# Kernel optimization log

Measured on AMD Instinct MI355X. Metric: run time of the kernel, lower is better.

## Reference

```python
import jax, jax.numpy as jnp
import numpy as np

N, E, S, G = 20000, 60000, 3000, 128
EAD = 5
DIMS = [(16, 32), (32, 64), (64, 64)]  # NNConv (M_in, M_out) per layer
HID = 128  # edge-MLP hidden
FC_IN = 64 + 8  # conv output + raw continuous feats


def setup_inputs() -> dict:
    key = jax.random.key(0)
    ks = iter(jax.random.split(key, 64))
    inp = {}
    inp['x'] = jax.random.normal(next(ks), (N, 24), jnp.float32)
    inp['edge_index'] = jax.random.randint(next(ks), (2, E), 0, N)
    inp['edge_attr'] = jax.random.uniform(next(ks), (E, EAD), jnp.float32)
    inp['node_to_subgraph'] = jnp.sort(jax.random.randint(next(ks), (N,), 0, S))
    inp['subgraph_to_graph'] = jnp.sort(jax.random.randint(next(ks), (S,), 0, G))
    for i, (mi, mo) in enumerate(DIMS):
        inp[f'conv{i}_w1'] = jax.random.normal(next(ks), (EAD, HID), jnp.float32) / np.sqrt(EAD)
        inp[f'conv{i}_b1'] = jnp.zeros((HID,), jnp.float32)
        inp[f'conv{i}_w2'] = jax.random.normal(next(ks), (HID, mi * mo), jnp.float32) / np.sqrt(HID * mi)
        inp[f'conv{i}_b2'] = jnp.zeros((mi * mo,), jnp.float32)
        inp[f'conv{i}_root'] = jax.random.normal(next(ks), (mi, mo), jnp.float32) / np.sqrt(mi)
        inp[f'conv{i}_bias'] = jnp.zeros((mo,), jnp.float32)
    dims_fc = [(FC_IN, FC_IN // 2), (FC_IN // 2, FC_IN // 4), (FC_IN // 4, 1)]
    for i, (di, do) in enumerate(dims_fc):
        inp[f'fc{i+1}_w'] = jax.random.normal(next(ks), (di, do), jnp.float32) / np.sqrt(di)
        inp[f'fc{i+1}_b'] = jnp.zeros((do,), jnp.float32)
    return inp


def _nnconv(x, src, dst, ea, w1, b1, w2, b2, root, bias):
    # edge MLP -> per-edge weight matrix [E, M_in, M_out]
    h = jax.nn.relu(ea @ w1 + b1)
    mi, mo = root.shape
    W = (h @ w2 + b2).reshape(-1, mi, mo)
    msg = jnp.einsum('ei,eio->eo', x[src], W)  # gather + per-edge matmul
    agg = jax.ops.segment_sum(msg, dst, num_segments=x.shape[0])  # scatter-add
    return agg + x @ root + bias


def _mean_pool(x, seg, num):
    s = jax.ops.segment_sum(x, seg, num_segments=num)
    c = jax.ops.segment_sum(jnp.ones((x.shape[0], 1), x.dtype), seg, num_segments=num)
    return s / jnp.maximum(c, 1.0)


def _forward(x, edge_index, edge_attr, node_to_subgraph, subgraph_to_graph, convs, fcs):
    src, dst = edge_index[0], edge_index[1]
    xi = x[:, :16]
    for p in convs:
        xi = jax.nn.elu(_nnconv(xi, src, dst, edge_attr, *p))
    x_cont = x[:, 16:]
    xc = jnp.concatenate([xi, x_cont], axis=1)  # [N, 72]
    xs = _mean_pool(xc, node_to_subgraph, S)    # [S, 72]
    xg = _mean_pool(xs, subgraph_to_graph, G)   # [G, 72]
    (w1, b1), (w2, b2), (w3, b3) = fcs
    xg = jax.nn.elu(xg @ w1 + b1)
    xg = jax.nn.elu(xg @ w2 + b2)
    return (xg @ w3 + b3).reshape(-1)


def reference(x, edge_index, edge_attr, node_to_subgraph, subgraph_to_graph,
              conv0_w1, conv0_b1, conv0_w2, conv0_b2, conv0_root, conv0_bias,
              conv1_w1, conv1_b1, conv1_w2, conv1_b2, conv1_root, conv1_bias,
              conv2_w1, conv2_b1, conv2_w2, conv2_b2, conv2_root, conv2_bias,
              fc1_w, fc1_b, fc2_w, fc2_b, fc3_w, fc3_b):
    convs = [
        (conv0_w1, conv0_b1, conv0_w2, conv0_b2, conv0_root, conv0_bias),
        (conv1_w1, conv1_b1, conv1_w2, conv1_b2, conv1_root, conv1_bias),
        (conv2_w1, conv2_b1, conv2_w2, conv2_b2, conv2_root, conv2_bias),
    ]
    fcs = [(fc1_w, fc1_b), (fc2_w, fc2_b), (fc3_w, fc3_b)]
    return _forward(x, edge_index, edge_attr, node_to_subgraph, subgraph_to_graph, convs, fcs)
```

## Files before the change

kernel.cpp:

```cpp
#include <hip/hip_runtime.h>
#include <hip/hip_bf16.h>
#include <cmath>

#define NN 20000
#define NE 60000
#define NS 3000
#define NG 128
#define HIDN 128
#define SCB 79

typedef float f32x16 __attribute__((ext_vector_type(16)));
typedef _Float16 f16x8 __attribute__((ext_vector_type(8)));

__device__ __forceinline__ float eluf(float v) { return v > 0.f ? v : expm1f(v); }

__device__ __forceinline__ void gload_lds16(const void* g, void* l) {
    __builtin_amdgcn_global_load_lds(
        (const __attribute__((address_space(1))) unsigned int*)g,
        (__attribute__((address_space(3))) unsigned int*)l, 16, 0, 0);
}

__device__ __forceinline__ void vmwait0() {
    asm volatile("s_waitcnt vmcnt(0)" ::: "memory");
}
__device__ __forceinline__ void vmwait8() {
    asm volatile("s_waitcnt vmcnt(8)" ::: "memory");
}

__global__ void k_hist(const int* __restrict__ dst, int* __restrict__ deg) {
    int e = blockIdx.x * 256 + threadIdx.x;
    if (e < NE) atomicAdd(&deg[dst[e]], 1);
}

__global__ void k_scan1(const int* __restrict__ deg, int* __restrict__ bsum) {
    __shared__ int s[256];
    const int t = threadIdx.x;
    int i = blockIdx.x * 256 + t;
    s[t] = (i < NN) ? deg[i] : 0;
    __syncthreads();
#pragma unroll
    for (int off = 128; off > 0; off >>= 1) {
        if (t < off) s[t] += s[t + off];
        __syncthreads();
    }
    if (t == 0) bsum[blockIdx.x] = s[0];
}

__global__ void k_scan2(const int* __restrict__ bsum, int* __restrict__ boff) {
    __shared__ int s[SCB];
    const int t = threadIdx.x;
    if (t < SCB) s[t] = bsum[t];
    __syncthreads();
    if (t == 0) {
        int acc = 0;
        for (int i = 0; i < SCB; ++i) { int v = s[i]; s[i] = acc; acc += v; }
    }
    __syncthreads();
    if (t < SCB) boff[t] = s[t];
}

__global__ void k_scan3(const int* __restrict__ deg, const int* __restrict__ boff,
                        int* __restrict__ rowptr) {
    __shared__ int s[256];
    const int t = threadIdx.x;
    int i = blockIdx.x * 256 + t;
    int v = (i < NN) ? deg[i] : 0;
    s[t] = v;
    __syncthreads();
#pragma unroll
    for (int off = 1; off < 256; off <<= 1) {
        int a = (t >= off) ? s[t - off] : 0;
        __syncthreads();
        s[t] += a;
        __syncthreads();
    }
    if (i < NN) rowptr[i + 1] = boff[blockIdx.x] + s[t];
    if (i == 0) rowptr[0] = 0;
}

__global__ void k_scatter(const int* __restrict__ src, const int* __restrict__ dst,
                          const int* __restrict__ rowptr, int* __restrict__ tmp,
                          int* __restrict__ eord, int* __restrict__ srcS) {
    int e = blockIdx.x * 256 + threadIdx.x;
    if (e >= NE) return;
    int d = dst[e];
    int pos = rowptr[d] + atomicAdd(&tmp[d], 1);
    eord[pos] = e;
    srcS[pos] = src[e];
}

#define PRE_N0 66048
#define PRE_N1 264192
#define PRE_N2 528384
#define PRE_N3 320000
#define PRE_TOT (PRE_N0 + PRE_N1 + PRE_N2 + PRE_N3)

__global__ void k_prep(const float* __restrict__ w20, const float* __restrict__ b20,
                       const float* __restrict__ w21, const float* __restrict__ b21,
                       const float* __restrict__ w22, const float* __restrict__ b22,
                       const float* __restrict__ x,
                       _Float16* __restrict__ w2t0, _Float16* __restrict__ w2t1,
                       _Float16* __restrict__ w2t2, _Float16* __restrict__ x16h) {
    int idx = blockIdx.x * 256 + threadIdx.x;
    if (idx < PRE_N0) {
        constexpr int KP = 129 * 16, KF = 128 * 16, MO = 32;
        int o = idx / KP, kg = idx % KP;
        float v = (kg < KF) ? w20[(size_t)kg * MO + o] : b20[(kg - KF) * MO + o];
        w2t0[idx] = (_Float16)v;
    } else if (idx < PRE_N0 + PRE_N1) {
        int i2 = idx - PRE_N0;
        constexpr int KP = 129 * 32, KF = 128 * 32, MO = 64;
        int o = i2 / KP, kg = i2 % KP;
        float v = (kg < KF) ? w21[(size_t)kg * MO + o] : b21[(kg - KF) * MO + o];
        w2t1[i2] = (_Float16)v;
    } else if (idx < PRE_N0 + PRE_N1 + PRE_N2) {
        int i2 = idx - PRE_N0 - PRE_N1;
        constexpr int KP = 129 * 64, KF = 128 * 64, MO = 64;
        int o = i2 / KP, kg = i2 % KP;
        float v = (kg < KF) ? w22[(size_t)kg * MO + o] : b22[(kg - KF) * MO + o];
        w2t2[i2] = (_Float16)v;
    } else if (idx < PRE_TOT) {
        int i2 = idx - PRE_N0 - PRE_N1 - PRE_N2;
        int n = i2 >> 4, i = i2 & 15;
        x16h[i2] = (_Float16)x[n * 24 + i];
    }
}

template <int MI, int MO, int XS>
__global__ __launch_bounds__(256, 2) void k_edgeB(
    const _Float16* __restrict__ xi, const float* __restrict__ ea,
    const float* __restrict__ w1, const float* __restrict__ b1,
    const _Float16* __restrict__ w2t, const int* __restrict__ srcS,
    const int* __restrict__ eord, _Float16* __restrict__ msg) {
    constexpr int PH  = MI / 16;
    constexpr int KP  = 129 * MI;
    constexpr int NT  = MO / 32;
    constexpr int CH  = 16 / (PH * NT);
    constexpr int NCH = 64 / CH;
    static_assert(CH * PH * NT == 16, "ITEMS must be 16");
    static_assert(NCH % 2 == 0, "chunk loop unrolled x2");

    __shared__ __align__(16) _Float16 sb[2][2][16 * 512];

    const int lane = threadIdx.x & 63;
    const int w    = threadIdx.x >> 6;
    const int mg   = w & 1;
    const int kh   = w >> 1;
    const int lo5  = lane & 31;
    const int hi   = lane >> 5;
    const int e0   = blockIdx.x * 128 + mg * 64;
    const int kb   = kh * 64;

    const int rc0 = min(e0 + lo5, NE - 1);
    const int rc1 = min(e0 + 32 + lo5, NE - 1);
    const int s0 = srcS[rc0];
    const int s1 = srcS[rc1];

    float ea0[5], ea1[5];
    {
        const int eo0 = eord[rc0], eo1 = eord[rc1];
#pragma unroll
        for (int d = 0; d < 5; ++d) {
            ea0[d] = ea[eo0 * 5 + d];
            ea1[d] = ea[eo1 * 5 + d];
        }
    }

    f16x8 xr0[PH], xr1[PH];
    {
        const _Float16* xb0 = xi + (size_t)s0 * XS + hi * 8;
        const _Float16* xb1 = xi + (size_t)s1 * XS + hi * 8;
#pragma unroll
        for (int p = 0; p < PH; ++p) {
            xr0[p] = *reinterpret_cast<const f16x8*>(xb0 + p * 16);
            xr1[p] = *reinterpret_cast<const f16x8*>(xb1 + p * 16);
        }
    }

    f32x16 acc[2][NT];
#pragma unroll
    for (int m = 0; m < 2; ++m)
#pragma unroll
        for (int n = 0; n < NT; ++n)
#pragma unroll
            for (int i = 0; i < 16; ++i) acc[m][n][i] = 0.f;

    auto stage = [&](int buf, int kc) {
#pragma unroll
        for (int jj = 0; jj < 8; ++jj) {
            const int j  = mg + jj * 2;
            const int n  = j % NT;
            const int kp = j / NT;
            const int p  = kp % PH;
            const int kk = kp / PH;
            gload_lds16(w2t + (size_t)(n * 32 + lo5) * KP
                            + (size_t)(kb + kc + kk) * MI + p * 16 + hi * 8,
                        &sb[kh][buf][j * 512]);
        }
    };

    auto calc_h = [&](int kc, _Float16* h0, _Float16* h1) {
#pragma unroll
        for (int kk = 0; kk < CH; ++kk) {
            const int k = kb + kc + kk;
            const float c0 = w1[0 * HIDN + k], c1 = w1[1 * HIDN + k],
                        c2 = w1[2 * HIDN + k], c3 = w1[3 * HIDN + k],
                        c4 = w1[4 * HIDN + k], bb = b1[k];
            float t0 = bb, t1 = bb;
            t0 = fmaf(ea0[0], c0, t0); t1 = fmaf(ea1[0], c0, t1);
            t0 = fmaf(ea0[1], c1, t0); t1 = fmaf(ea1[1], c1, t1);
            t0 = fmaf(ea0[2], c2, t0); t1 = fmaf(ea1[2], c2, t1);
            t0 = fmaf(ea0[3], c3, t0); t1 = fmaf(ea1[3], c3, t1);
            t0 = fmaf(ea0[4], c4, t0); t1 = fmaf(ea1[4], c4, t1);
            h0[kk] = (_Float16)fmaxf(t0, 0.f);
            h1[kk] = (_Float16)fmaxf(t1, 0.f);
        }
    };

    auto compute = [&](int buf, const _Float16* h0, const _Float16* h1) {
        const _Float16* sbc = &sb[kh][buf][0];
#pragma unroll
        for (int kk = 0; kk < CH; ++kk) {
            const _Float16 hv0 = h0[kk];
            const _Float16 hv1 = h1[kk];
            const f16x8 h80 = {hv0, hv0, hv0, hv0, hv0, hv0, hv0, hv0};
            const f16x8 h81 = {hv1, hv1, hv1, hv1, hv1, hv1, hv1, hv1};
#pragma unroll
            for (int p = 0; p < PH; ++p) {
                const f16x8 af0 = xr0[p] * h80;
                const f16x8 af1 = xr1[p] * h81;
#pragma unroll
                for (int n = 0; n < NT; ++n) {
                    const f16x8 bv = *reinterpret_cast<const f16x8*>(
                        &sbc[((kk * PH + p) * NT + n) * 512 + lane * 8]);
                    acc[0][n] = __builtin_amdgcn_mfma_f32_32x32x16_f16(af0, bv, acc[0][n], 0, 0, 0);
                    acc[1][n] = __builtin_amdgcn_mfma_f32_32x32x16_f16(af1, bv, acc[1][n], 0, 0, 0);
                }
            }
        }
    };

    _Float16 hA0[CH], hA1[CH], hB0[CH], hB1[CH];

    stage(0, 0);
    calc_h(0, hA0, hA1);

    for (int c = 0; c < NCH; c += 2) {
        stage(1, (c + 1) * CH);
        calc_h((c + 1) * CH, hB0, hB1);
        vmwait8();
        __builtin_amdgcn_sched_barrier(0);
        __builtin_amdgcn_s_barrier();
        __builtin_amdgcn_sched_barrier(0);
        compute(0, hA0, hA1);
        __builtin_amdgcn_sched_barrier(0);
        __builtin_amdgcn_s_barrier();

        const bool pf = (c + 2 < NCH);
        if (pf) {
            stage(0, (c + 2) * CH);
            calc_h((c + 2) * CH, hA0, hA1);
            vmwait8();
        } else {
            vmwait0();
        }
        __builtin_amdgcn_sched_barrier(0);
        __builtin_amdgcn_s_barrier();
        __builtin_amdgcn_sched_barrier(0);
        compute(1, hB0, hB1);
        __builtin_amdgcn_sched_barrier(0);
        __builtin_amdgcn_s_barrier();
    }

    if (kh == 1) {
#pragma unroll
        for (int p = 0; p < PH; ++p) {
#pragma unroll
            for (int n = 0; n < NT; ++n) {
                const f16x8 bv = *reinterpret_cast<const f16x8*>(
                    w2t + (size_t)(n * 32 + lo5) * KP + (size_t)128 * MI + p * 16 + hi * 8);
                acc[0][n] = __builtin_amdgcn_mfma_f32_32x32x16_f16(xr0[p], bv, acc[0][n], 0, 0, 0);
                acc[1][n] = __builtin_amdgcn_mfma_f32_32x32x16_f16(xr1[p], bv, acc[1][n], 0, 0, 0);
            }
        }
    }

    __syncthreads();
    float* red = reinterpret_cast<float*>(&sb[0][0][0]);
    if (kh == 1) {
#pragma unroll
        for (int m = 0; m < 2; ++m)
#pragma unroll
            for (int n = 0; n < NT; ++n) {
                float* d = red + (size_t)((mg * 2 + m) * NT + n) * 1024 + lane;
#pragma unroll
                for (int i = 0; i < 16; ++i) d[i * 64] = acc[m][n][i];
            }
    }
    __syncthreads();
    if (kh == 0) {
#pragma unroll
        for (int m = 0; m < 2; ++m)
#pragma unroll
            for (int n = 0; n < NT; ++n) {
                const float* s = red + (size_t)((mg * 2 + m) * NT + n) * 1024 + lane;
#pragma unroll
                for (int i = 0; i < 16; ++i) acc[m][n][i] += s[i * 64];
            }
#pragma unroll
        for (int m = 0; m < 2; ++m)
#pragma unroll
            for (int q = 0; q < 4; ++q)
#pragma unroll
                for (int a2 = 0; a2 < 4; ++a2) {
                    const int e = e0 + m * 32 + 4 * hi + 8 * q + a2;
                    if (e < NE) {
#pragma unroll
                        for (int n = 0; n < NT; ++n)
                            msg[(size_t)e * MO + n * 32 + lo5] =
                                (_Float16)acc[m][n][4 * q + a2];
                    }
                }
    }
}

template <int MI, int MO, int XS>
__global__ void k_agg(const _Float16* __restrict__ msg, const int* __restrict__ rowptr,
                      const float* __restrict__ xi, const float* __restrict__ root,
                      const float* __restrict__ bias, float* __restrict__ out,
                      _Float16* __restrict__ outh) {
    int idx = blockIdx.x * 256 + threadIdx.x;
    if (idx >= NN * MO) return;
    int n = idx / MO, o = idx % MO;
    float s = bias[o];
#pragma unroll
    for (int i = 0; i < MI; ++i) s = fmaf(xi[(size_t)n * XS + i], root[i * MO + o], s);
    const int j0 = rowptr[n], j1 = rowptr[n + 1];
    for (int j = j0; j < j1; ++j) s += (float)msg[(size_t)j * MO + o];
    float r = eluf(s);
    out[idx] = r;
    outh[idx] = (_Float16)r;
}

__global__ void k_agg_pool(const _Float16* __restrict__ msg, const int* __restrict__ rowptr,
                           const float* __restrict__ xi, const float* __restrict__ root,
                           const float* __restrict__ bias, const float* __restrict__ x,
                           const int* __restrict__ n2s, float* __restrict__ xs_sum,
                           float* __restrict__ cs) {
    int idx = blockIdx.x * 256 + threadIdx.x;
    if (idx >= NN * 72) return;
    int n = idx / 72, o = idx % 72;
    float r;
    if (o < 64) {
        float s = bias[o];
#pragma unroll
        for (int i = 0; i < 64; ++i) s = fmaf(xi[(size_t)n * 64 + i], root[i * 64 + o], s);
        const int j0 = rowptr[n], j1 = rowptr[n + 1];
        for (int j = j0; j < j1; ++j) s += (float)msg[(size_t)j * 64 + o];
        r = eluf(s);
    } else {
        r = x[n * 24 + 16 + (o - 64)];
    }
    const int sg = n2s[n];
    atomicAdd(&xs_sum[sg * 72 + o], r);
    if (o == 0) atomicAdd(&cs[sg], 1.f);
}

__global__ void k_pool_g(const float* __restrict__ xs_sum, const float* __restrict__ cs,
                         const int* __restrict__ s2g, float* __restrict__ xg_sum,
                         float* __restrict__ cg) {
    int idx = blockIdx.x * 256 + threadIdx.x;
    if (idx >= NS * 72) return;
    int s = idx / 72, j = idx % 72;
    float v = xs_sum[s * 72 + j] / fmaxf(cs[s], 1.f);
    int g = s2g[s];
    atomicAdd(&xg_sum[g * 72 + j], v);
    if (j == 0) atomicAdd(&cg[g], 1.f);
}

__global__ void k_fc(const float* __restrict__ xg_sum, const float* __restrict__ cg,
                     const float* __restrict__ w1, const float* __restrict__ b1,
                     const float* __restrict__ w2, const float* __restrict__ b2,
                     const float* __restrict__ w3, const float* __restrict__ b3,
                     float* __restrict__ out) {
    int g = threadIdx.x;
    if (g >= NG) return;
    float inv = 1.f / fmaxf(cg[g], 1.f);
    float v[72];
#pragma unroll
    for (int j = 0; j < 72; ++j) v[j] = xg_sum[g * 72 + j] * inv;
    float h1[36];
#pragma unroll
    for (int o = 0; o < 36; ++o) {
        float s = b1[o];
#pragma unroll
        for (int i = 0; i < 72; ++i) s = fmaf(v[i], w1[i * 36 + o], s);
        h1[o] = eluf(s);
    }
    float h2[18];
#pragma unroll
    for (int o = 0; o < 18; ++o) {
        float s = b2[o];
#pragma unroll
        for (int i = 0; i < 36; ++i) s = fmaf(h1[i], w2[i * 18 + o], s);
        h2[o] = eluf(s);
    }
    float s = b3[0];
#pragma unroll
    for (int i = 0; i < 18; ++i) s = fmaf(h2[i], w3[i], s);
    out[g] = s;
}

extern "C" void kernel_launch(void* const* d_in, const int* in_sizes, int n_in,
                              void* d_out, int out_size, void* d_ws, size_t ws_size,
                              hipStream_t stream) {
    const float* x   = (const float*)d_in[0];
    const int*   ei  = (const int*)d_in[1];
    const float* ea  = (const float*)d_in[2];
    const int*   n2s = (const int*)d_in[3];
    const int*   s2g = (const int*)d_in[4];
    const int* src = ei;
    const int* dst = ei + NE;

    const float* cw1[3]   = {(const float*)d_in[5],  (const float*)d_in[11], (const float*)d_in[17]};
    const float* cb1[3]   = {(const float*)d_in[6],  (const float*)d_in[12], (const float*)d_in[18]};
    const float* cw2[3]   = {(const float*)d_in[7],  (const float*)d_in[13], (const float*)d_in[19]};
    const float* cb2[3]   = {(const float*)d_in[8],  (const float*)d_in[14], (const float*)d_in[20]};
    const float* croot[3] = {(const float*)d_in[9],  (const float*)d_in[15], (const float*)d_in[21]};
    const float* cbias[3] = {(const float*)d_in[10], (const float*)d_in[16], (const float*)d_in[22]};
    const float* fc1w = (const float*)d_in[23];
    const float* fc1b = (const float*)d_in[24];
    const float* fc2w = (const float*)d_in[25];
    const float* fc2b = (const float*)d_in[26];
    const float* fc3w = (const float*)d_in[27];
    const float* fc3b = (const float*)d_in[28];

    char* W = (char*)d_ws;
    float*    xiA   = (float*)(W);
    float*    xiB   = (float*)(W + 5120000);
    _Float16* xiAh  = (_Float16*)(W + 10240000);
    _Float16* xiBh  = (_Float16*)(W + 12800000);
    _Float16* x16h  = (_Float16*)(W + 15360000);
    _Float16* msg   = (_Float16*)(W + 16000000);
    float*    xs_sum= (float*)(W + 23680000);
    float*    cs    = (float*)(W + 24544000);
    float*    xg_sum= (float*)(W + 24556000);
    float*    cg    = (float*)(W + 24592864);
    int*      deg   = (int*)(W + 24593376);
    int*      tmp   = (int*)(W + 24673376);
    _Float16* w2t0  = (_Float16*)(W + 24753376);
    _Float16* w2t1  = (_Float16*)(W + 24885472);
    _Float16* w2t2  = (_Float16*)(W + 25413856);
    int*      rowptr= (int*)(W + 26470624);
    int*      eord  = (int*)(W + 26550640);
    int*      srcS  = (int*)(W + 26790640);
    int*      bsum  = (int*)(W + 27030640);
    int*      boff  = (int*)(W + 27030960);

    hipMemsetAsync(xs_sum, 0, 1073376, stream);

    k_hist<<<(NE + 255) / 256, 256, 0, stream>>>(dst, deg);
    k_scan1<<<SCB, 256, 0, stream>>>(deg, bsum);
    k_scan2<<<1, 128, 0, stream>>>(bsum, boff);
    k_scan3<<<SCB, 256, 0, stream>>>(deg, boff, rowptr);
    k_scatter<<<(NE + 255) / 256, 256, 0, stream>>>(src, dst, rowptr, tmp, eord, srcS);

    k_prep<<<(PRE_TOT + 255) / 256, 256, 0, stream>>>(
        cw2[0], cb2[0], cw2[1], cb2[1], cw2[2], cb2[2], x, w2t0, w2t1, w2t2, x16h);

    const int EB = (NE + 127) / 128;

    k_edgeB<16, 32, 16><<<EB, 256, 0, stream>>>(x16h, ea, cw1[0], cb1[0], w2t0, srcS, eord, msg);
    k_agg<16, 32, 24><<<(NN * 32 + 255) / 256, 256, 0, stream>>>(msg, rowptr, x, croot[0], cbias[0], xiB, xiBh);

    k_edgeB<32, 64, 32><<<EB, 256, 0, stream>>>(xiBh, ea, cw1[1], cb1[1], w2t1, srcS, eord, msg);
    k_agg<32, 64, 32><<<(NN * 64 + 255) / 256, 256, 0, stream>>>(msg, rowptr, xiB, croot[1], cbias[1], xiA, xiAh);

    k_edgeB<64, 64, 64><<<EB, 256, 0, stream>>>(xiAh, ea, cw1[2], cb1[2], w2t2, srcS, eord, msg);
    k_agg_pool<<<(NN * 72 + 255) / 256, 256, 0, stream>>>(msg, rowptr, xiA, croot[2], cbias[2],
                                                          x, n2s, xs_sum, cs);

    k_pool_g<<<(NS * 72 + 255) / 256, 256, 0, stream>>>(xs_sum, cs, s2g, xg_sum, cg);
    k_fc<<<1, 128, 0, stream>>>(xg_sum, cg, fc1w, fc1b, fc2w, fc2b, fc3w, fc3b, (float*)d_out);
}
```

Measured before the change: 302.0 us.

## Split layer-3 edge kernel over hidden-dim slices with partial message buffers

```diff
diff --git a/kernel.cpp b/kernel.cpp
--- a/kernel.cpp
+++ b/kernel.cpp
@@ -8,6 +8,8 @@
 #define NG 128
 #define HIDN 128
 #define SCB 79
+#define TILES 938
+#define SLST 3840000
 
 typedef float f32x16 __attribute__((ext_vector_type(16)));
 typedef _Float16 f16x8 __attribute__((ext_vector_type(8)));
@@ -325,6 +327,134 @@
 }
 
 template <int MI, int MO, int XS>
+__global__ __launch_bounds__(768, 3) void k_edgeP(
+    const _Float16* __restrict__ xi, const float* __restrict__ ea,
+    const float* __restrict__ w1, const float* __restrict__ b1,
+    const _Float16* __restrict__ w2t, const int* __restrict__ srcS,
+    const int* __restrict__ eord, _Float16* __restrict__ msgP, int tilesPerBlock) {
+    constexpr int PH = MI / 16;
+    constexpr int KP = 129 * MI;
+    constexpr int NT = MO / 32;
+    constexpr int MAXITEMS = 17 * PH * NT;
+
+    __shared__ __align__(16) _Float16 sb[MAXITEMS * 512];
+
+    const int t    = threadIdx.x;
+    const int lane = t & 63;
+    const int w    = t >> 6;
+    const int lo5  = lane & 31;
+    const int hi   = lane >> 5;
+
+    const int sl    = blockIdx.y;
+    const int k0    = sl * 16;
+    const int kspan = (sl == 7) ? 17 : 16;
+    const int items = kspan * PH * NT;
+
+    for (int j = w; j < items; j += 12) {
+        const int kk  = j / (PH * NT);
+        const int rem = j % (PH * NT);
+        const int p   = rem / NT;
+        const int n   = rem % NT;
+        gload_lds16(w2t + (size_t)(n * 32 + lo5) * KP
+                        + (size_t)(k0 + kk) * MI + p * 16 + hi * 8,
+                    &sb[j * 512]);
+    }
+    vmwait0();
+    __syncthreads();
+
+    _Float16* msgS = msgP + (size_t)sl * SLST;
+    const int tile0 = blockIdx.x * tilesPerBlock;
+    const int tile1 = min(tile0 + tilesPerBlock, TILES);
+
+    for (int tile = tile0 + w; tile < tile1; tile += 12) {
+        const int e0  = tile * 64;
+        const int rc0 = min(e0 + lo5, NE - 1);
+        const int rc1 = min(e0 + 32 + lo5, NE - 1);
+        const int s0 = srcS[rc0];
+        const int s1 = srcS[rc1];
+
+        float ea0[5], ea1[5];
+        {
+            const int eo0 = eord[rc0], eo1 = eord[rc1];
+#pragma unroll
+            for (int d = 0; d < 5; ++d) {
+                ea0[d] = ea[eo0 * 5 + d];
+                ea1[d] = ea[eo1 * 5 + d];
+            }
+        }
+
+        f16x8 xr0[PH], xr1[PH];
+        {
+            const _Float16* xb0 = xi + (size_t)s0 * XS + hi * 8;
+            const _Float16* xb1 = xi + (size_t)s1 * XS + hi * 8;
+#pragma unroll
+            for (int p = 0; p < PH; ++p) {
+                xr0[p] = *reinterpret_cast<const f16x8*>(xb0 + p * 16);
+                xr1[p] = *reinterpret_cast<const f16x8*>(xb1 + p * 16);
+            }
+        }
+
+        f32x16 acc[2][NT];
+#pragma unroll
+        for (int m = 0; m < 2; ++m)
+#pragma unroll
+            for (int n = 0; n < NT; ++n)
+#pragma unroll
+                for (int i = 0; i < 16; ++i) acc[m][n][i] = 0.f;
+
+        for (int kk2 = 0; kk2 < kspan; ++kk2) {
+            const int k = k0 + kk2;
+            _Float16 hv0, hv1;
+            if (k < 128) {
+                const float c0 = w1[0 * HIDN + k], c1 = w1[1 * HIDN + k],
+                            c2 = w1[2 * HIDN + k], c3 = w1[3 * HIDN + k],
+                            c4 = w1[4 * HIDN + k], bb = b1[k];
+                float t0 = bb, t1 = bb;
+                t0 = fmaf(ea0[0], c0, t0); t1 = fmaf(ea1[0], c0, t1);
+                t0 = fmaf(ea0[1], c1, t0); t1 = fmaf(ea1[1], c1, t1);
+                t0 = fmaf(ea0[2], c2, t0); t1 = fmaf(ea1[2], c2, t1);
+                t0 = fmaf(ea0[3], c3, t0); t1 = fmaf(ea1[3], c3, t1);
+                t0 = fmaf(ea0[4], c4, t0); t1 = fmaf(ea1[4], c4, t1);
+                hv0 = (_Float16)fmaxf(t0, 0.f);
+                hv1 = (_Float16)fmaxf(t1, 0.f);
+            } else {
+                hv0 = (_Float16)1.0f;
+                hv1 = (_Float16)1.0f;
+            }
+            const f16x8 h80 = {hv0, hv0, hv0, hv0, hv0, hv0, hv0, hv0};
+            const f16x8 h81 = {hv1, hv1, hv1, hv1, hv1, hv1, hv1, hv1};
+#pragma unroll
+            for (int p = 0; p < PH; ++p) {
+                const f16x8 af0 = xr0[p] * h80;
+                const f16x8 af1 = xr1[p] * h81;
+#pragma unroll
+                for (int n = 0; n < NT; ++n) {
+                    const f16x8 bv = *reinterpret_cast<const f16x8*>(
+                        &sb[((kk2 * PH + p) * NT + n) * 512 + lane * 8]);
+                    acc[0][n] = __builtin_amdgcn_mfma_f32_32x32x16_f16(af0, bv, acc[0][n], 0, 0, 0);
+                    acc[1][n] = __builtin_amdgcn_mfma_f32_32x32x16_f16(af1, bv, acc[1][n], 0, 0, 0);
+                }
+            }
+        }
+
+#pragma unroll
+        for (int m = 0; m < 2; ++m)
+#pragma unroll
+            for (int q = 0; q < 4; ++q)
+#pragma unroll
+                for (int a2 = 0; a2 < 4; ++a2) {
+                    const int e = e0 + m * 32 + 4 * hi + 8 * q + a2;
+                    if (e < NE) {
+#pragma unroll
+                        for (int n = 0; n < NT; ++n)
+                            msgS[(size_t)e * MO + n * 32 + lo5] =
+                                (_Float16)acc[m][n][4 * q + a2];
+                    }
+                }
+    }
+}
+
+template <int MI, int MO, int XS>
 __global__ void k_agg(const _Float16* __restrict__ msg, const int* __restrict__ rowptr,
                       const float* __restrict__ xi, const float* __restrict__ root,
                       const float* __restrict__ bias, float* __restrict__ out,
@@ -342,7 +472,8 @@
     outh[idx] = (_Float16)r;
 }
 
-__global__ void k_agg_pool(const _Float16* __restrict__ msg, const int* __restrict__ rowptr,
+__global__ void k_agg_pool(const _Float16* __restrict__ msgP, int nsl,
+                           const int* __restrict__ rowptr,
                            const float* __restrict__ xi, const float* __restrict__ root,
                            const float* __restrict__ bias, const float* __restrict__ x,
                            const int* __restrict__ n2s, float* __restrict__ xs_sum,
@@ -356,7 +487,10 @@
 #pragma unroll
         for (int i = 0; i < 64; ++i) s = fmaf(xi[(size_t)n * 64 + i], root[i * 64 + o], s);
         const int j0 = rowptr[n], j1 = rowptr[n + 1];
-        for (int j = j0; j < j1; ++j) s += (float)msg[(size_t)j * 64 + o];
+        for (int j = j0; j < j1; ++j) {
+            const _Float16* mp = msgP + (size_t)j * 64 + o;
+            for (int sl = 0; sl < nsl; ++sl) s += (float)mp[(size_t)sl * SLST];
+        }
         r = eluf(s);
     } else {
         r = x[n * 24 + 16 + (o - 64)];
@@ -441,21 +575,24 @@
     _Float16* xiAh  = (_Float16*)(W + 10240000);
     _Float16* xiBh  = (_Float16*)(W + 12800000);
     _Float16* x16h  = (_Float16*)(W + 15360000);
-    _Float16* msg   = (_Float16*)(W + 16000000);
-    float*    xs_sum= (float*)(W + 23680000);
-    float*    cs    = (float*)(W + 24544000);
-    float*    xg_sum= (float*)(W + 24556000);
-    float*    cg    = (float*)(W + 24592864);
-    int*      deg   = (int*)(W + 24593376);
-    int*      tmp   = (int*)(W + 24673376);
-    _Float16* w2t0  = (_Float16*)(W + 24753376);
-    _Float16* w2t1  = (_Float16*)(W + 24885472);
-    _Float16* w2t2  = (_Float16*)(W + 25413856);
-    int*      rowptr= (int*)(W + 26470624);
-    int*      eord  = (int*)(W + 26550640);
-    int*      srcS  = (int*)(W + 26790640);
-    int*      bsum  = (int*)(W + 27030640);
-    int*      boff  = (int*)(W + 27030960);
+    float*    xs_sum= (float*)(W + 16000000);
+    float*    cs    = (float*)(W + 16864000);
+    float*    xg_sum= (float*)(W + 16876000);
+    float*    cg    = (float*)(W + 16912864);
+    int*      deg   = (int*)(W + 16913376);
+    int*      tmp   = (int*)(W + 16993376);
+    _Float16* w2t0  = (_Float16*)(W + 17073376);
+    _Float16* w2t1  = (_Float16*)(W + 17205472);
+    _Float16* w2t2  = (_Float16*)(W + 17733856);
+    int*      rowptr= (int*)(W + 18790624);
+    int*      eord  = (int*)(W + 18870640);
+    int*      srcS  = (int*)(W + 19110640);
+    int*      bsum  = (int*)(W + 19350640);
+    int*      boff  = (int*)(W + 19350960);
+    _Float16* msgP  = (_Float16*)(W + 19351296);
+    const size_t NEED_P = 19351296ull + 8ull * 7680000ull;
+    const bool useP = (ws_size >= NEED_P);
+    _Float16* msg = msgP;
 
     hipMemsetAsync(xs_sum, 0, 1073376, stream);
 
@@ -476,9 +613,18 @@
     k_edgeB<32, 64, 32><<<EB, 256, 0, stream>>>(xiBh, ea, cw1[1], cb1[1], w2t1, srcS, eord, msg);
     k_agg<32, 64, 32><<<(NN * 64 + 255) / 256, 256, 0, stream>>>(msg, rowptr, xiB, croot[1], cbias[1], xiA, xiAh);
 
-    k_edgeB<64, 64, 64><<<EB, 256, 0, stream>>>(xiAh, ea, cw1[2], cb1[2], w2t2, srcS, eord, msg);
-    k_agg_pool<<<(NN * 72 + 255) / 256, 256, 0, stream>>>(msg, rowptr, xiA, croot[2], cbias[2],
-                                                          x, n2s, xs_sum, cs);
+    if (useP) {
+        const int XB = 32;
+        const int TPB = (TILES + XB - 1) / XB;
+        k_edgeP<64, 64, 64><<<dim3(XB, 8), 768, 0, stream>>>(
+            xiAh, ea, cw1[2], cb1[2], w2t2, srcS, eord, msgP, TPB);
+        k_agg_pool<<<(NN * 72 + 255) / 256, 256, 0, stream>>>(
+            msgP, 8, rowptr, xiA, croot[2], cbias[2], x, n2s, xs_sum, cs);
+    } else {
+        k_edgeB<64, 64, 64><<<EB, 256, 0, stream>>>(xiAh, ea, cw1[2], cb1[2], w2t2, srcS, eord, msg);
+        k_agg_pool<<<(NN * 72 + 255) / 256, 256, 0, stream>>>(
+            msg, 1, rowptr, xiA, croot[2], cbias[2], x, n2s, xs_sum, cs);
+    }
 
     k_pool_g<<<(NS * 72 + 255) / 256, 256, 0, stream>>>(xs_sum, cs, s2g, xg_sum, cg);
     k_fc<<<1, 128, 0, stream>>>(xg_sum, cg, fc1w, fc1b, fc2w, fc2b, fc3w, fc3b, (float*)d_out);
```

Measured after the change: 302.0 us. About the same (+0.0%).
